# Kernel optimization log

Measured on AMD Instinct MI355X. Metric: run time of the kernel, lower is better.

The kernel has to match this reference:

```python
import jax, jax.numpy as jnp
import numpy as np

B, N, H, L = 4096, 512, 1024, 8


def setup_inputs() -> dict:
    key = jax.random.key(0)
    k1, k2, k3, k4 = jax.random.split(key, 4)
    x = jax.random.normal(k1, (B, N), dtype=jnp.float32)
    beta = jax.random.uniform(k2, (H, L, N), dtype=jnp.float32)  # torch.rand init
    bound = 1.0 / np.sqrt(N)
    W = jax.random.uniform(k3, (H, N), minval=-bound, maxval=bound, dtype=jnp.float32)
    b = jax.random.uniform(k4, (H,), minval=-bound, maxval=bound, dtype=jnp.float32)
    return {"x": x, "beta": beta, "W": W, "b": b}


def reference(x, beta, W, b):
    # Original computes c[h,j,k] = sum_l beta[h,l,j]*beta[h,l,k], then
    # out_fm[b,h] = sum_{j<k} x[b,j]*x[b,k]*c[h,j,k]  (strict upper-tri mask).
    # FM identity: sum_{j<k} x_j x_k <v_j, v_k>
    #            = 0.5 * sum_l [ (sum_j x_j v_{lj})^2 - sum_j x_j^2 v_{lj}^2 ]
    s = jnp.einsum('bn,hln->bhl', x, beta)            # (B, H, L)
    ssq = jnp.einsum('bn,hln->bhl', x * x, beta * beta)  # (B, H, L)
    fm = 0.5 * jnp.sum(s * s - ssq, axis=-1)          # (B, H)
    linear_out = x @ W.T + b                          # (B, H)
    return fm + linear_out
```

## Files before the change

kernel.cpp:

```cpp
#include <hip/hip_runtime.h>
#include <stdint.h>

static constexpr int B_DIM = 4096;
static constexpr int N_DIM = 512;
static constexpr int H_DIM = 1024;
static constexpr int L_DIM = 8;
static constexpr int HL    = H_DIM * L_DIM;
static constexpr int KC    = 2 * N_DIM;

typedef __attribute__((ext_vector_type(8))) short short8;
typedef __attribute__((ext_vector_type(4))) float f32x4;

#define BM 128
#define BN 128
#define BK 32

__device__ __forceinline__ uint16_t f2bf(float f) {
  uint32_t u = __float_as_uint(f);
  u += 0x7fffu + ((u >> 16) & 1u);
  return (uint16_t)(u >> 16);
}

__device__ __forceinline__ void stage16(const uint16_t* g, uint16_t* l) {
  __builtin_amdgcn_global_load_lds(
      (const __attribute__((address_space(1))) void*)g,
      (__attribute__((address_space(3))) void*)l, 16, 0, 0);
}

__global__ void prep_x_kernel(const float* __restrict__ x, uint16_t* __restrict__ xcomb) {
  int idx = blockIdx.x * blockDim.x + threadIdx.x;
  int b = idx >> 9, n = idx & 511;
  float v = x[idx];
  xcomb[(size_t)b * KC + n]         = f2bf(v);
  xcomb[(size_t)b * KC + N_DIM + n] = f2bf(v * v);
}

__global__ void prep_beta_kernel(const float* __restrict__ beta, uint16_t* __restrict__ bb) {
  int idx = blockIdx.x * blockDim.x + threadIdx.x;
  bb[idx] = f2bf(beta[idx]);
}

__global__ void prep_w_kernel(const float* __restrict__ W, const float* __restrict__ beta,
                              uint16_t* __restrict__ combW) {
  int idx = blockIdx.x * blockDim.x + threadIdx.x;
  int h = idx >> 9, n = idx & 511;
  combW[(size_t)h * KC + n] = f2bf(W[idx]);
  float s = 0.f;
#pragma unroll
  for (int l = 0; l < L_DIM; ++l) {
    float v = beta[((size_t)h * L_DIM + l) * N_DIM + n];
    s += v * v;
  }
  combW[(size_t)h * KC + N_DIM + n] = f2bf(-0.5f * s);
}

template <int KTOT, bool FM>
__global__ __launch_bounds__(256) void gemm_kernel(
    const uint16_t* __restrict__ A,
    const uint16_t* __restrict__ Bt,
    const float* __restrict__ bias,
    float* __restrict__ out)
{
  constexpr int LDA = KC;
  constexpr int LDB = FM ? N_DIM : KC;

  __shared__ __align__(16) uint16_t As[BM * BK];
  __shared__ __align__(16) uint16_t Bs[BN * BK];

  const int tid  = threadIdx.x;
  const int lane = tid & 63;
  const int wave = tid >> 6;
  const int wm = wave >> 1, wn = wave & 1;

  const int row0 = blockIdx.y * BM;
  const int col0 = blockIdx.x * BN;

  f32x4 acc[4][4] = {};

  const int m0 = tid >> 2, kq0 = (tid & 3) * 8;
  const int m1 = (tid + 256) >> 2;

  for (int kt = 0; kt < KTOT; kt += BK) {
    stage16(A + (size_t)(row0 + m0) * LDA + kt + kq0, As + tid * 8);
    stage16(A + (size_t)(row0 + m1) * LDA + kt + kq0, As + (tid + 256) * 8);
    stage16(Bt + (size_t)(col0 + m0) * LDB + kt + kq0, Bs + tid * 8);
    stage16(Bt + (size_t)(col0 + m1) * LDB + kt + kq0, Bs + (tid + 256) * 8);
    __syncthreads();

    const int fr = lane & 15;
    const int ko = (lane >> 4) * 8;
    short8 af[4], bfr[4];
#pragma unroll
    for (int i = 0; i < 4; ++i)
      af[i] = *(const short8*)(As + (wm * 64 + i * 16 + fr) * BK + ko);
#pragma unroll
    for (int j = 0; j < 4; ++j)
      bfr[j] = *(const short8*)(Bs + (wn * 64 + j * 16 + fr) * BK + ko);
#pragma unroll
    for (int i = 0; i < 4; ++i)
#pragma unroll
      for (int j = 0; j < 4; ++j)
        acc[i][j] = __builtin_amdgcn_mfma_f32_16x16x32_bf16(af[i], bfr[j], acc[i][j], 0, 0, 0);
    __syncthreads();
  }

  const int cfr  = lane & 15;
  const int quad = lane >> 4;
  if (FM) {
    const int hcol0 = blockIdx.x * (BN / L_DIM);
#pragma unroll
    for (int i = 0; i < 4; ++i) {
#pragma unroll
      for (int j = 0; j < 4; ++j) {
        const int h_in = wn * 8 + j * 2 + (cfr >> 3);
        const int rowb = row0 + wm * 64 + i * 16 + quad * 4;
#pragma unroll
        for (int r = 0; r < 4; ++r) {
          float v = acc[i][j][r];
          v = v * v;
          v += __shfl_xor(v, 1);
          v += __shfl_xor(v, 2);
          v += __shfl_xor(v, 4);
          if ((lane & 7) == 0)
            out[(size_t)(rowb + r) * H_DIM + hcol0 + h_in] = 0.5f * v;
        }
      }
    }
  } else {
#pragma unroll
    for (int i = 0; i < 4; ++i) {
#pragma unroll
      for (int j = 0; j < 4; ++j) {
        const int col  = col0 + wn * 64 + j * 16 + cfr;
        const int rowb = row0 + wm * 64 + i * 16 + quad * 4;
        const float bs = bias[col];
#pragma unroll
        for (int r = 0; r < 4; ++r) {
          size_t o = (size_t)(rowb + r) * H_DIM + col;
          out[o] += acc[i][j][r] + bs;
        }
      }
    }
  }
}

extern "C" void kernel_launch(void* const* d_in, const int* in_sizes, int n_in,
                              void* d_out, int out_size, void* d_ws, size_t ws_size,
                              hipStream_t stream) {
  const float* x    = (const float*)d_in[0];
  const float* beta = (const float*)d_in[1];
  const float* W    = (const float*)d_in[2];
  const float* bias = (const float*)d_in[3];
  float* out = (float*)d_out;

  uint16_t* xcomb = (uint16_t*)d_ws;
  uint16_t* betab = xcomb + (size_t)B_DIM * KC;
  uint16_t* combW = betab + (size_t)HL * N_DIM;

  prep_x_kernel<<<B_DIM * N_DIM / 256, 256, 0, stream>>>(x, xcomb);
  prep_beta_kernel<<<HL * N_DIM / 256, 256, 0, stream>>>(beta, betab);
  prep_w_kernel<<<H_DIM * N_DIM / 256, 256, 0, stream>>>(W, beta, combW);

  gemm_kernel<N_DIM, true><<<dim3(HL / BN, B_DIM / BM), 256, 0, stream>>>(
      xcomb, betab, nullptr, out);
  gemm_kernel<KC, false><<<dim3(H_DIM / BN, B_DIM / BM), 256, 0, stream>>>(
      xcomb, combW, bias, out);
}
```

Baseline: 172.2 us.

## Fuse prep kernels, XOR-swizzle LDS tiles, and shrink linear GEMM tile

Merges the three bf16 conversion kernels into one launch to cut launch overhead. Applies an XOR swizzle to the 16-byte chunks in the LDS A/B tiles so the MFMA fragment reads hit fewer bank conflicts. Templates the GEMM on tile size and runs the linear GEMM with 128x64 tiles to get more blocks across the CUs, at the cost of less reuse per block.

```diff
diff --git a/kernel.cpp b/kernel.cpp
--- a/kernel.cpp
+++ b/kernel.cpp
@@ -11,8 +11,6 @@
 typedef __attribute__((ext_vector_type(8))) short short8;
 typedef __attribute__((ext_vector_type(4))) float f32x4;
 
-#define BM 128
-#define BN 128
 #define BK 32
 
 __device__ __forceinline__ uint16_t f2bf(float f) {
@@ -27,22 +25,24 @@
       (__attribute__((address_space(3))) void*)l, 16, 0, 0);
 }
 
-__global__ void prep_x_kernel(const float* __restrict__ x, uint16_t* __restrict__ xcomb) {
-  int idx = blockIdx.x * blockDim.x + threadIdx.x;
-  int b = idx >> 9, n = idx & 511;
-  float v = x[idx];
-  xcomb[(size_t)b * KC + n]         = f2bf(v);
-  xcomb[(size_t)b * KC + N_DIM + n] = f2bf(v * v);
-}
-
-__global__ void prep_beta_kernel(const float* __restrict__ beta, uint16_t* __restrict__ bb) {
-  int idx = blockIdx.x * blockDim.x + threadIdx.x;
-  bb[idx] = f2bf(beta[idx]);
-}
-
-__global__ void prep_w_kernel(const float* __restrict__ W, const float* __restrict__ beta,
-                              uint16_t* __restrict__ combW) {
-  int idx = blockIdx.x * blockDim.x + threadIdx.x;
+__global__ void prep_kernel(const float* __restrict__ x, const float* __restrict__ beta,
+                            const float* __restrict__ W,
+                            uint16_t* __restrict__ xcomb, uint16_t* __restrict__ betab,
+                            uint16_t* __restrict__ combW) {
+  int idx = blockIdx.x * 256 + threadIdx.x;
+  if (idx < HL * N_DIM) {
+    betab[idx] = f2bf(beta[idx]);
+    return;
+  }
+  idx -= HL * N_DIM;
+  if (idx < B_DIM * N_DIM) {
+    int b = idx >> 9, n = idx & 511;
+    float v = x[idx];
+    xcomb[(size_t)b * KC + n]         = f2bf(v);
+    xcomb[(size_t)b * KC + N_DIM + n] = f2bf(v * v);
+    return;
+  }
+  idx -= B_DIM * N_DIM;
   int h = idx >> 9, n = idx & 511;
   combW[(size_t)h * KC + n] = f2bf(W[idx]);
   float s = 0.f;
@@ -54,7 +54,7 @@
   combW[(size_t)h * KC + N_DIM + n] = f2bf(-0.5f * s);
 }
 
-template <int KTOT, bool FM>
+template <int BM_, int BN_, int KTOT, bool FM>
 __global__ __launch_bounds__(256) void gemm_kernel(
     const uint16_t* __restrict__ A,
     const uint16_t* __restrict__ Bt,
@@ -63,57 +63,69 @@
 {
   constexpr int LDA = KC;
   constexpr int LDB = FM ? N_DIM : KC;
+  constexpr int MI  = BM_ / 32;
+  constexpr int NJ  = BN_ / 32;
+  constexpr int CHA = BM_ * BK / 8;
+  constexpr int CHB = BN_ * BK / 8;
 
-  __shared__ __align__(16) uint16_t As[BM * BK];
-  __shared__ __align__(16) uint16_t Bs[BN * BK];
+  __shared__ __align__(16) uint16_t As[BM_ * BK];
+  __shared__ __align__(16) uint16_t Bs[BN_ * BK];
 
   const int tid  = threadIdx.x;
   const int lane = tid & 63;
   const int wave = tid >> 6;
   const int wm = wave >> 1, wn = wave & 1;
 
-  const int row0 = blockIdx.y * BM;
-  const int col0 = blockIdx.x * BN;
+  const int row0 = blockIdx.y * BM_;
+  const int col0 = blockIdx.x * BN_;
 
-  f32x4 acc[4][4] = {};
+  f32x4 acc[MI][NJ] = {};
 
-  const int m0 = tid >> 2, kq0 = (tid & 3) * 8;
-  const int m1 = (tid + 256) >> 2;
+  const int fr   = lane & 15;
+  const int quad = lane >> 4;
 
   for (int kt = 0; kt < KTOT; kt += BK) {
-    stage16(A + (size_t)(row0 + m0) * LDA + kt + kq0, As + tid * 8);
-    stage16(A + (size_t)(row0 + m1) * LDA + kt + kq0, As + (tid + 256) * 8);
-    stage16(Bt + (size_t)(col0 + m0) * LDB + kt + kq0, Bs + tid * 8);
-    stage16(Bt + (size_t)(col0 + m1) * LDB + kt + kq0, Bs + (tid + 256) * 8);
+#pragma unroll
+    for (int s = tid; s < CHA; s += 256) {
+      int m = s >> 2, cp = s & 3, c = cp ^ ((m >> 1) & 3);
+      stage16(A + (size_t)(row0 + m) * LDA + kt + c * 8, As + s * 8);
+    }
+#pragma unroll
+    for (int s = tid; s < CHB; s += 256) {
+      int m = s >> 2, cp = s & 3, c = cp ^ ((m >> 1) & 3);
+      stage16(Bt + (size_t)(col0 + m) * LDB + kt + c * 8, Bs + s * 8);
+    }
     __syncthreads();
 
-    const int fr = lane & 15;
-    const int ko = (lane >> 4) * 8;
-    short8 af[4], bfr[4];
+    short8 af[MI], bfr[NJ];
 #pragma unroll
-    for (int i = 0; i < 4; ++i)
-      af[i] = *(const short8*)(As + (wm * 64 + i * 16 + fr) * BK + ko);
+    for (int i = 0; i < MI; ++i) {
+      int m = wm * (BM_ / 2) + i * 16 + fr;
+      int cp = quad ^ ((m >> 1) & 3);
+      af[i] = *(const short8*)(As + (m * 4 + cp) * 8);
+    }
 #pragma unroll
-    for (int j = 0; j < 4; ++j)
-      bfr[j] = *(const short8*)(Bs + (wn * 64 + j * 16 + fr) * BK + ko);
+    for (int j = 0; j < NJ; ++j) {
+      int m = wn * (BN_ / 2) + j * 16 + fr;
+      int cp = quad ^ ((m >> 1) & 3);
+      bfr[j] = *(const short8*)(Bs + (m * 4 + cp) * 8);
+    }
 #pragma unroll
-    for (int i = 0; i < 4; ++i)
+    for (int i = 0; i < MI; ++i)
 #pragma unroll
-      for (int j = 0; j < 4; ++j)
+      for (int j = 0; j < NJ; ++j)
         acc[i][j] = __builtin_amdgcn_mfma_f32_16x16x32_bf16(af[i], bfr[j], acc[i][j], 0, 0, 0);
     __syncthreads();
   }
 
-  const int cfr  = lane & 15;
-  const int quad = lane >> 4;
   if (FM) {
-    const int hcol0 = blockIdx.x * (BN / L_DIM);
+    const int hcol0 = blockIdx.x * (BN_ / L_DIM);
 #pragma unroll
-    for (int i = 0; i < 4; ++i) {
+    for (int i = 0; i < MI; ++i) {
 #pragma unroll
-      for (int j = 0; j < 4; ++j) {
-        const int h_in = wn * 8 + j * 2 + (cfr >> 3);
-        const int rowb = row0 + wm * 64 + i * 16 + quad * 4;
+      for (int j = 0; j < NJ; ++j) {
+        const int h_in = wn * (BN_ / 16) + j * 2 + (fr >> 3);
+        const int rowb = row0 + wm * (BM_ / 2) + i * 16 + quad * 4;
 #pragma unroll
         for (int r = 0; r < 4; ++r) {
           float v = acc[i][j][r];
@@ -128,11 +140,11 @@
     }
   } else {
 #pragma unroll
-    for (int i = 0; i < 4; ++i) {
+    for (int i = 0; i < MI; ++i) {
 #pragma unroll
-      for (int j = 0; j < 4; ++j) {
-        const int col  = col0 + wn * 64 + j * 16 + cfr;
-        const int rowb = row0 + wm * 64 + i * 16 + quad * 4;
+      for (int j = 0; j < NJ; ++j) {
+        const int col  = col0 + wn * (BN_ / 2) + j * 16 + fr;
+        const int rowb = row0 + wm * (BM_ / 2) + i * 16 + quad * 4;
         const float bs = bias[col];
 #pragma unroll
         for (int r = 0; r < 4; ++r) {
@@ -157,12 +169,11 @@
   uint16_t* betab = xcomb + (size_t)B_DIM * KC;
   uint16_t* combW = betab + (size_t)HL * N_DIM;
 
-  prep_x_kernel<<<B_DIM * N_DIM / 256, 256, 0, stream>>>(x, xcomb);
-  prep_beta_kernel<<<HL * N_DIM / 256, 256, 0, stream>>>(beta, betab);
-  prep_w_kernel<<<H_DIM * N_DIM / 256, 256, 0, stream>>>(W, beta, combW);
+  const int prep_elems = HL * N_DIM + B_DIM * N_DIM + H_DIM * N_DIM;
+  prep_kernel<<<(prep_elems + 255) / 256, 256, 0, stream>>>(x, beta, W, xcomb, betab, combW);
 
-  gemm_kernel<N_DIM, true><<<dim3(HL / BN, B_DIM / BM), 256, 0, stream>>>(
+  gemm_kernel<128, 128, N_DIM, true><<<dim3(HL / 128, B_DIM / 128), 256, 0, stream>>>(
       xcomb, betab, nullptr, out);
-  gemm_kernel<KC, false><<<dim3(H_DIM / BN, B_DIM / BM), 256, 0, stream>>>(
+  gemm_kernel<128, 64, KC, false><<<dim3(H_DIM / 64, B_DIM / 128), 256, 0, stream>>>(
       xcomb, combW, bias, out);
 }
```

After: 165.6 us. -3.8%, faster.
